# Optimization experiments

Measured on AMD Instinct MI355X. Metric: run time of the kernel, lower is better.

The kernel has to match this reference:

```python
import jax, jax.numpy as jnp
import numpy as np

DIM = 128          # feature dim
HID = 512          # rnn hidden dim
NC = 128           # n_comps (MLP outputs 2*NC)
N = 512            # batch
IN = 2 * DIM + 1   # rnn input size
MLP_H = 4 * HID


def setup_inputs() -> dict:
    key = jax.random.key(0)
    ks = jax.random.split(key, 16)
    s_in = 1.0 / np.sqrt(IN)
    s_h = 1.0 / np.sqrt(HID)
    s_m = 1.0 / np.sqrt(MLP_H)
    f32 = jnp.float32
    return {
        "x": jax.random.normal(ks[0], (N, DIM), f32),
        "mask": jnp.zeros((DIM,), f32),  # all dims unobserved
        # RNN layer 0 (input 2*dim+1 -> hidden)
        "W_ih0": jax.random.uniform(ks[1], (HID, IN), f32, -s_in, s_in),
        "W_hh0": jax.random.uniform(ks[2], (HID, HID), f32, -s_h, s_h),
        "b_ih0": jax.random.uniform(ks[3], (HID,), f32, -s_h, s_h),
        "b_hh0": jax.random.uniform(ks[4], (HID,), f32, -s_h, s_h),
        # RNN layer 1 (hidden -> hidden)
        "W_ih1": jax.random.uniform(ks[5], (HID, HID), f32, -s_h, s_h),
        "W_hh1": jax.random.uniform(ks[6], (HID, HID), f32, -s_h, s_h),
        "b_ih1": jax.random.uniform(ks[7], (HID,), f32, -s_h, s_h),
        "b_hh1": jax.random.uniform(ks[8], (HID,), f32, -s_h, s_h),
        # MLP: hidden -> 4*hidden -> 2*n_comps (ReLU)
        "W1": jax.random.uniform(ks[9], (MLP_H, HID), f32, -s_h, s_h),
        "b1": jax.random.uniform(ks[10], (MLP_H,), f32, -s_h, s_h),
        "W2": jax.random.uniform(ks[11], (2 * NC, MLP_H), f32, -s_m, s_m),
        "b2": jax.random.uniform(ks[12], (2 * NC,), f32, -s_m, s_m),
    }


def _log_prob(xt, means, covs):
    # xt: [N,1], means/covs: [N,NC]
    prec = jax.lax.rsqrt(jax.nn.softplus(covs))
    quad = jnp.sum((xt - means) ** 2 / (prec * prec), axis=1, keepdims=True)
    log_det = jnp.sum(jnp.log(prec), axis=1, keepdims=True)
    return -0.5 * (DIM * np.log(2.0 * np.pi) + quad) + log_det


def reference(x, mask, W_ih0, W_hh0, b_ih0, b_hh0, W_ih1, W_hh1, b_ih1, b_hh1,
              W1, b1, W2, b2):
    n = x.shape[0]
    x_o = x * mask                       # [N, DIM]
    masks = jnp.broadcast_to(mask, (n, DIM))
    # mask is all-zeros by construction -> every dim is unobserved, in order
    x_u = x                              # [N, DIM] unobserved values

    # previous unobserved value fed at each step (zeros at step 0)
    prev_seq = jnp.concatenate([jnp.zeros((n, 1), x.dtype), x_u[:, :-1]], axis=1)
    xs = (prev_seq.T[:, :, None], x_u.T[:, :, None])  # each [DIM, N, 1]

    def step(carry, inp):
        h0, h1, p, _ = carry
        prev_col, targ_col = inp
        cat = jnp.concatenate([prev_col, x_o, masks], axis=1)  # [N, 2*DIM+1]
        h0 = jnp.tanh(cat @ W_ih0.T + b_ih0 + h0 @ W_hh0.T + b_hh0)
        h1 = jnp.tanh(h0 @ W_ih1.T + b_ih1 + h1 @ W_hh1.T + b_hh1)
        o = h1                                               # [N, HID]
        hid = jax.nn.relu(o @ W1.T + b1)
        mc = hid @ W2.T + b2                                 # [N, 2*NC]
        means, covs = mc[:, :NC], mc[:, NC:]
        p = p + _log_prob(targ_col, means, covs)
        return (h0, h1, p, o), None

    init = (jnp.zeros((n, HID), x.dtype), jnp.zeros((n, HID), x.dtype),
            jnp.zeros((n, 1), x.dtype), jnp.zeros((n, HID), x.dtype))
    (h0, h1, p, o_last), _ = jax.lax.scan(step, init, xs)
    return o_last[:, None, :], p  # o: [N,1,HID], p: [N,1]
```

## Files before the change

kernel.cpp:

```cpp
#include <hip/hip_runtime.h>

typedef _Float16 f16;
typedef _Float16 f16x8 __attribute__((ext_vector_type(8)));
typedef float    f32x4 __attribute__((ext_vector_type(4)));
typedef unsigned int u32;
typedef u32 u32x4 __attribute__((ext_vector_type(4)));

#define MFMA16(a, b, c) __builtin_amdgcn_mfma_f32_16x16x32_f16((a), (b), (c), 0, 0, 0)

#define HSZ 262144
#define LOGDET_C 235.2482644923962f

__device__ __forceinline__ void ld16_s(u32x4& d, const f16* p) {
    asm volatile("global_load_dwordx4 %0, %1, off sc0 sc1" : "=v"(d) : "v"(p));
}
__device__ __forceinline__ void ldf_n(float& d, const float* p) {
    asm volatile("global_load_dword %0, %1, off" : "=v"(d) : "v"(p));
}
__device__ __forceinline__ void st2_n(f16* p, f16 v) {
    u32 u = (u32)__builtin_bit_cast(unsigned short, v);
    asm volatile("global_store_short %0, %1, off" :: "v"(p), "v"(u) : "memory");
}
__device__ __forceinline__ void st2_s(f16* p, f16 v) {
    u32 u = (u32)__builtin_bit_cast(unsigned short, v);
    asm volatile("global_store_short %0, %1, off sc0 sc1" :: "v"(p), "v"(u) : "memory");
}
__device__ __forceinline__ void sti_s(int* p, int v) {
    asm volatile("global_store_dword %0, %1, off sc0 sc1" :: "v"(p), "v"(v) : "memory");
}
__device__ __forceinline__ int ldi_s(const int* p) {
    int v;
    asm volatile("global_load_dword %0, %1, off sc0 sc1\ns_waitcnt vmcnt(0)"
                 : "=v"(v) : "v"(p) : "memory");
    return v;
}
__device__ __forceinline__ void gl16(const f16* g, char* l) {
    __builtin_amdgcn_global_load_lds(
        (const __attribute__((address_space(1))) u32*)g,
        (__attribute__((address_space(3))) u32*)l, 16, 0, 0);
}
__device__ __forceinline__ float tanh_fast(float x) {
    float e = __builtin_amdgcn_exp2f(x * 2.8853900817779268f);
    return 1.f - 2.f * __builtin_amdgcn_rcpf(e + 1.f);
}

__global__ void k_conv(const float* __restrict__ x, const float* __restrict__ mask,
                       const float* __restrict__ Wih0,
                       const float* __restrict__ b_ih0, const float* __restrict__ b_hh0,
                       const float* __restrict__ Whh0, const float* __restrict__ Wih1,
                       const float* __restrict__ Whh1, const float* __restrict__ W1,
                       const float* __restrict__ W2,
                       f16* __restrict__ A, f16* __restrict__ B1,
                       float* __restrict__ biasv,
                       f16* __restrict__ Whh0h, f16* __restrict__ Wih1h,
                       f16* __restrict__ Whh1h, f16* __restrict__ W1h,
                       f16* __restrict__ W2h, f16* __restrict__ h1all,
                       int* __restrict__ slots, int* __restrict__ xcdtab)
{
    int gid = blockIdx.x * 256 + threadIdx.x;
    {
        int c = gid >> 7, k = gid & 127;
        A[gid]  = (f16)(x[gid] * mask[k]);
        B1[gid] = (f16)Wih0[c * 257 + 1 + k];
    }
    if (gid < 512) {
        float s = b_ih0[gid] + b_hh0[gid];
        const float* wrow = Wih0 + gid * 257 + 129;
        for (int k = 0; k < 128; k++) s += mask[k] * wrow[k];
        biasv[gid] = s;
    }
    for (int i = gid; i < 262144; i += 65536) {
        Whh0h[i] = (f16)Whh0[i];
        Wih1h[i] = (f16)Wih1[i];
        Whh1h[i] = (f16)Whh1[i];
        h1all[i] = (f16)0.f;
    }
    for (int i = gid; i < 1048576; i += 65536) W1h[i] = (f16)W1[i];
    for (int i = gid; i < 524288;  i += 65536) W2h[i] = (f16)W2[i];
    if (gid < 32768) slots[gid] = 0;
    if (gid < 4096)  xcdtab[gid] = -1;
}

__global__ __launch_bounds__(256) void k_base(const f16* __restrict__ A,
                                              const f16* __restrict__ B1,
                                              const float* __restrict__ biasv,
                                              float* __restrict__ base,
                                              f16* __restrict__ h0s0)
{
    __shared__ float part[4][32][32];
    int tid = threadIdx.x;
    int w = tid >> 6, l = tid & 63;
    int R0 = (blockIdx.x >> 4) * 32, C0 = (blockIdx.x & 15) * 32;
    int lr = l & 15, hi = l >> 4;

    const f16* a0p = A  + (R0 + lr) * 128 + w * 32 + hi * 8;
    const f16* b0p = B1 + (C0 + lr) * 128 + w * 32 + hi * 8;
    f16x8 a0 = *(const f16x8*)(a0p);
    f16x8 a1 = *(const f16x8*)(a0p + 16 * 128);
    f16x8 b0 = *(const f16x8*)(b0p);
    f16x8 b1 = *(const f16x8*)(b0p + 16 * 128);
    f32x4 z = {0.f, 0.f, 0.f, 0.f};
    f32x4 acc00 = MFMA16(a0, b0, z);
    f32x4 acc01 = MFMA16(a0, b1, z);
    f32x4 acc10 = MFMA16(a1, b0, z);
    f32x4 acc11 = MFMA16(a1, b1, z);
#pragma unroll
    for (int r = 0; r < 4; r++) {
        part[w][hi * 4 + r][lr]           = acc00[r];
        part[w][hi * 4 + r][16 + lr]      = acc01[r];
        part[w][16 + hi * 4 + r][lr]      = acc10[r];
        part[w][16 + hi * 4 + r][16 + lr] = acc11[r];
    }
    __syncthreads();
    int rr = tid >> 3, c0 = (tid & 7) * 4;
    int gr = R0 + rr;
#pragma unroll
    for (int cc = 0; cc < 4; cc++) {
        int gc = C0 + c0 + cc;
        float s = part[0][rr][c0 + cc] + part[1][rr][c0 + cc] +
                  part[2][rr][c0 + cc] + part[3][rr][c0 + cc] + biasv[gc];
        base[gr * 512 + gc] = s;
        h0s0[gr * 512 + gc] = (f16)tanh_fast(s);
    }
}

#define LDH(off, f) (*(const f16x8*)((char*)Wl + (off) + lrowB + \
        ((((f) * 64 + hi16)) ^ lswz)))
#define LDB(m, f) (*(const f16x8*)((char*)Wl + \
        (((m) * 32768 + colL * 1024 + (f) * 64 + hi16) ^ cswz)))

#define RNN_STAGED(ST2x)                                                      \
    for (int p = 0; p < 128; p++) {                                           \
        const f16* H0 = h0all + (size_t)(p & PMASK) * HSZ;                    \
        const f16* H1 = h1all + (size_t)p * HSZ;                              \
        f16* H1o = h1all + (size_t)(p + 1) * HSZ;                             \
        f16* H0o = h0all + (size_t)((p + 1) & PMASK) * HSZ;                   \
        float xprev[4];                                                       \
        _Pragma("unroll")                                                     \
        for (int r = 0; r < 4; r++) ldf_n(xprev[r], x + (outrow + r) * 128 + p); \
        if (p) { int v; for (;;) { v = ldi_s(pollB); if (__all(v >= p)) break; \
                                   __builtin_amdgcn_s_sleep(1); } }           \
        _Pragma("unroll")                                                     \
        for (int i = 0; i < 8; i++) {                                         \
            int rr = w * 8 + i;                                               \
            gl16(H0 + (size_t)(R0 + rr) * 512 + ((l ^ (rr & 7)) * 8),         \
                 (char*)Wl + OFF_H0S + rr * 1024);                            \
        }                                                                     \
        asm volatile("s_waitcnt vmcnt(0)" ::: "memory");                      \
        __syncthreads();                                                      \
        f32x4 z4 = {0.f, 0.f, 0.f, 0.f};                                      \
        f32x4 a0a = z4, a0b = z4, a1a = z4, a1b = z4;                         \
        _Pragma("unroll")                                                     \
        for (int f = 0; f < 16; f += 2) {                                     \
            f16x8 A0 = LDH(OFF_H0S, f);                                       \
            f16x8 A1 = LDH(OFF_H0S, f + 1);                                   \
            a0a = MFMA16(A0, bW0[f],     a0a);                                \
            a0b = MFMA16(A1, bW0[f + 1], a0b);                                \
            a1a = MFMA16(A0, LDB(0, f),     a1a);                             \
            a1b = MFMA16(A1, LDB(0, f + 1), a1b);                             \
        }                                                                     \
        f32x4 acc0 = a0a + a0b;                                               \
        _Pragma("unroll")                                                     \
        for (int r = 0; r < 4; r++) {                                         \
            f16 v0 = (f16)tanh_fast(acc0[r] + basef[r] + xprev[r] * w0);      \
            ST2x(H0o + (outrow + r) * 512 + outcolg, v0);                     \
        }                                                                     \
        asm volatile("s_waitcnt vmcnt(0)" ::: "memory");                      \
        if (l == 0) sti_s(myB, p + 1);                                        \
        if (p) { int v; for (;;) { v = ldi_s(pollA); if (__all(v >= p)) break; \
                                   __builtin_amdgcn_s_sleep(1); } }           \
        _Pragma("unroll")                                                     \
        for (int i = 0; i < 8; i++) {                                         \
            int rr = w * 8 + i;                                               \
            gl16(H1 + (size_t)(R0 + rr) * 512 + ((l ^ (rr & 7)) * 8),         \
                 (char*)Wl + OFF_H1S + rr * 1024);                            \
        }                                                                     \
        asm volatile("s_waitcnt vmcnt(0)" ::: "memory");                      \
        __syncthreads();                                                      \
        _Pragma("unroll")                                                     \
        for (int f = 0; f < 16; f += 2) {                                     \
            f16x8 A0 = LDH(OFF_H1S, f);                                       \
            f16x8 A1 = LDH(OFF_H1S, f + 1);                                   \
            a1a = MFMA16(A0, LDB(1, f),     a1a);                             \
            a1b = MFMA16(A1, LDB(1, f + 1), a1b);                             \
        }                                                                     \
        f32x4 acc1 = a1a + a1b;                                               \
        _Pragma("unroll")                                                     \
        for (int r = 0; r < 4; r++) {                                         \
            f16 v1 = (f16)tanh_fast(acc1[r] + bsum);                          \
            ST2x(H1o + (outrow + r) * 512 + outcolg, v1);                     \
        }                                                                     \
        asm volatile("s_waitcnt vmcnt(0)" ::: "memory");                      \
        if (l == 0) sti_s(myA, p + 1);                                        \
    }

#define RNN_DIRECT()                                                          \
    for (int p = 0; p < 128; p++) {                                           \
        const f16* H0 = h0all + (size_t)(p & PMASK) * HSZ;                    \
        const f16* H1 = h1all + (size_t)p * HSZ;                              \
        const f16* ap = H0 + (R0 + r_lo + lr) * 512 + hi * 8;                 \
        const f16* bp = H1 + (R0 + r_lo + lr) * 512 + hi * 8;                 \
        f16* H1o = h1all + (size_t)(p + 1) * HSZ;                             \
        f16* H0o = h0all + (size_t)((p + 1) & PMASK) * HSZ;                   \
        float xprev[4];                                                       \
        _Pragma("unroll")                                                     \
        for (int r = 0; r < 4; r++) ldf_n(xprev[r], x + (outrow + r) * 128 + p); \
        if (p) { int v; for (;;) { v = ldi_s(pollB); if (__all(v >= p)) break; \
                                   __builtin_amdgcn_s_sleep(1); } }           \
        u32x4 ra0[16], ra1[16];                                               \
        __builtin_amdgcn_sched_barrier(0);                                    \
        _Pragma("unroll")                                                     \
        for (int f = 0; f < 16; f++) ld16_s(ra0[f], ap + f * 32);             \
        asm volatile("s_waitcnt vmcnt(0)" ::: "memory");                      \
        __builtin_amdgcn_sched_barrier(0);                                    \
        f32x4 z4 = {0.f, 0.f, 0.f, 0.f};                                      \
        f32x4 a0a = z4, a0b = z4, a1a = z4, a1b = z4;                         \
        _Pragma("unroll")                                                     \
        for (int f = 0; f < 16; f += 2) {                                     \
            f16x8 A0 = __builtin_bit_cast(f16x8, ra0[f]);                     \
            f16x8 A1 = __builtin_bit_cast(f16x8, ra0[f + 1]);                 \
            a0a = MFMA16(A0, bW0[f],     a0a);                                \
            a0b = MFMA16(A1, bW0[f + 1], a0b);                                \
            a1a = MFMA16(A0, LDB(0, f),     a1a);                             \
            a1b = MFMA16(A1, LDB(0, f + 1), a1b);                             \
        }                                                                     \
        f32x4 acc0 = a0a + a0b;                                               \
        _Pragma("unroll")                                                     \
        for (int r = 0; r < 4; r++) {                                         \
            f16 v0 = (f16)tanh_fast(acc0[r] + basef[r] + xprev[r] * w0);      \
            st2_s(H0o + (outrow + r) * 512 + outcolg, v0);                    \
        }                                                                     \
        asm volatile("s_waitcnt vmcnt(0)" ::: "memory");                      \
        if (l == 0) sti_s(myB, p + 1);                                        \
        if (p) { int v; for (;;) { v = ldi_s(pollA); if (__all(v >= p)) break; \
                                   __builtin_amdgcn_s_sleep(1); } }           \
        __builtin_amdgcn_sched_barrier(0);                                    \
        _Pragma("unroll")                                                     \
        for (int f = 0; f < 16; f++) ld16_s(ra1[f], bp + f * 32);             \
        asm volatile("s_waitcnt vmcnt(0)" ::: "memory");                      \
        __builtin_amdgcn_sched_barrier(0);                                    \
        _Pragma("unroll")                                                     \
        for (int f = 0; f < 16; f += 2) {                                     \
            a1a = MFMA16(__builtin_bit_cast(f16x8, ra1[f]),     LDB(1, f),     a1a); \
            a1b = MFMA16(__builtin_bit_cast(f16x8, ra1[f + 1]), LDB(1, f + 1), a1b); \
        }                                                                     \
        f32x4 acc1 = a1a + a1b;                                               \
        _Pragma("unroll")                                                     \
        for (int r = 0; r < 4; r++) {                                         \
            f16 v1 = (f16)tanh_fast(acc1[r] + bsum);                          \
            st2_s(H1o + (outrow + r) * 512 + outcolg, v1);                    \
        }                                                                     \
        asm volatile("s_waitcnt vmcnt(0)" ::: "memory");                      \
        if (l == 0) sti_s(myA, p + 1);                                        \
    }

template<bool H0F>
__global__ __launch_bounds__(256, 1) void k_rnn(
    f16* __restrict__ h0all, f16* __restrict__ h1all,
    const f16* __restrict__ Whh0h, const f16* __restrict__ Wih1h,
    const f16* __restrict__ Whh1h,
    const float* __restrict__ base, const float* __restrict__ x,
    const float* __restrict__ Wih0, const float* __restrict__ b_ih1,
    const float* __restrict__ b_hh1, int* __restrict__ slots,
    int* __restrict__ xcdtab)
{
    constexpr int PMASK = H0F ? 255 : 1;
    const int OFF_H0S = 65536, OFF_H1S = 98304;
    __shared__ __align__(16) char Wl[131072];
    __shared__ int s_fast;
    int tid = threadIdx.x;
    int w = tid >> 6, l = tid & 63;
    int bid = blockIdx.x;
    int sub = (bid >> 3) & 1, cj = bid >> 4;
    int cluster = (bid & 7) * 2 + sub;
    int R0 = cluster * 32, C0 = cj * 32;

    int xcdreg;
    asm("s_getreg_b32 %0, hwreg(20, 0, 4)" : "=s"(xcdreg));
    int my_xcd = xcdreg & 7;
    if (H0F && tid == 0) sti_s(xcdtab + (cluster * 16 + cj) * 16, my_xcd);

    {
        const f16* srcs[2] = { Wih1h, Whh1h };
        for (int m = 0; m < 2; m++) {
            const f16* S = srcs[m] + (size_t)C0 * 512;
            for (int cch = tid; cch < 2048; cch += 256) {
                int col = cch >> 6, kc = cch & 63;
                f16x8 v = *(const f16x8*)(S + col * 512 + kc * 8);
                int byte = m * 32768 + col * 1024 + kc * 16;
                byte ^= (col & 7) << 4;
                *(f16x8*)((char*)Wl + byte) = v;
            }
        }
    }
    __syncthreads();

    int lr = l & 15, hi = l >> 4;
    int r_lo = (w >> 1) * 16, c_lo = (w & 1) * 16;
    int outrow = R0 + r_lo + hi * 4;
    int outcolg = C0 + c_lo + lr;
    int colL = c_lo + lr;
    int lrow = r_lo + lr;
    int lrowB = lrow * 1024;
    int hi16 = hi * 16;
    int lswz = (lrow & 7) << 4;
    int cswz = (colL & 7) << 4;

    f16x8 bW0[16];
    {
        const f16* w0p = Whh0h + (size_t)outcolg * 512 + hi * 8;
#pragma unroll
        for (int f = 0; f < 16; f++) bW0[f] = *(const f16x8*)(w0p + f * 32);
    }

    float basef[4];
#pragma unroll
    for (int r = 0; r < 4; r++) basef[r] = base[(outrow + r) * 512 + outcolg];
    float w0 = Wih0[outcolg * 257];
    float bsum = b_ih1[outcolg] + b_hh1[outcolg];

    int* slotA = slots;
    int* slotB = slots + 16384;
    int wslot = cj * 4 + w;
    int* myA = slotA + (cluster * 64 + wslot) * 16;
    int* myB = slotB + (cluster * 64 + wslot) * 16;
    const int* pollA = slotA + (cluster * 64 + l) * 16;
    const int* pollB = slotB + (cluster * 64 + l) * 16;

    bool fast = false;
    if constexpr (H0F) {
        if (w == 0) {
            int v;
            for (;;) {
                v = (l < 16) ? ldi_s(xcdtab + (cluster * 16 + l) * 16) : 0;
                if (!__any(l < 16 && v == -1)) break;
                __builtin_amdgcn_s_sleep(1);
            }
            int f = __all(l >= 16 || v == my_xcd);
            if (l == 0) s_fast = f;
        }
        __syncthreads();
        fast = (s_fast != 0);
    } else {
        if (tid == 0) s_fast = 0;
        __syncthreads();
    }

    if (H0F && fast) {
        RNN_STAGED(st2_n)
    } else if (H0F) {
        RNN_STAGED(st2_s)
    } else {
        RNN_DIRECT()
    }
}
#undef LDH
#undef LDB

__global__ __launch_bounds__(512, 2) void k_phaseB(const f16* __restrict__ h1all,
                                                   const f16* __restrict__ W1h,
                                                   const f16* __restrict__ W2h,
                                                   const float* __restrict__ b1v,
                                                   const float* __restrict__ b2,
                                                   const float* __restrict__ x,
                                                   float* __restrict__ pcontrib)
{
    __shared__ __align__(16) char Wl[108544];
    const int OFF_W2 = 65536, OFF_HID = 98304;

    int tid = threadIdx.x;
    int wv = tid >> 6, l = tid & 63;
    int lr = l & 15, hi = l >> 4;
    int M0 = blockIdx.x * 128;

    const f16* Hrow = h1all + HSZ + (size_t)(M0 + wv * 16 + lr) * 512;
    f16x8 afrag[16];
#pragma unroll
    for (int ks = 0; ks < 16; ks++)
        afrag[ks] = *(const f16x8*)(Hrow + ks * 32 + hi * 8);

    f32x4 mc[16] = {};

    {
#pragma unroll
        for (int it = 0; it < 4; it++) {
            int idx = it * 512 + tid;
            gl16(W1h + (size_t)(idx & 31) * 512 + (idx >> 5) * 8,
                 Wl + idx * 16);
        }
#pragma unroll
        for (int it = 0; it < 2; it++) {
            int idx = it * 512 + tid;
            gl16(W2h + (size_t)(idx & 255) * 2048 + (idx >> 8) * 8,
                 Wl + OFF_W2 + idx * 16);
        }
    }

    for (int c = 0; c < 64; c++) {
        int p = c & 1;
        __syncthreads();

        if (c + 1 < 64) {
            const int nc = (c + 1) * 32, q = p ^ 1;
#pragma unroll
            for (int it = 0; it < 4; it++) {
                int idx = it * 512 + tid;
                gl16(W1h + (size_t)(nc + (idx & 31)) * 512 + (idx >> 5) * 8,
                     Wl + q * 32768 + idx * 16);
            }
#pragma unroll
            for (int it = 0; it < 2; it++) {
                int idx = it * 512 + tid;
                gl16(W2h + (size_t)(idx & 255) * 2048 + nc + (idx >> 8) * 8,
                     Wl + OFF_W2 + q * 16384 + idx * 16);
            }
        }

        {
            f32x4 s3a = {0.f, 0.f, 0.f, 0.f}, s3b = s3a;
#pragma unroll
            for (int ks = 0; ks < 16; ks++) {
                f16x8 wb0 = *(const f16x8*)(Wl + p * 32768 +
                                            ((ks * 4 + hi) * 32 + lr) * 16);
                f16x8 wb1 = *(const f16x8*)(Wl + p * 32768 +
                                            ((ks * 4 + hi) * 32 + 16 + lr) * 16);
                s3a = MFMA16(afrag[ks], wb0, s3a);
                s3b = MFMA16(afrag[ks], wb1, s3b);
            }
            float bb0 = b1v[c * 32 + lr];
            float bb1 = b1v[c * 32 + 16 + lr];
#pragma unroll
            for (int r = 0; r < 4; r++) {
                int lrow = wv * 16 + hi * 4 + r;
                *(f16*)(Wl + OFF_HID + (lrow * 40 + lr) * 2) =
                    (f16)fmaxf(s3a[r] + bb0, 0.f);
                *(f16*)(Wl + OFF_HID + (lrow * 40 + 16 + lr) * 2) =
                    (f16)fmaxf(s3b[r] + bb1, 0.f);
            }
        }
        __syncthreads();

        {
            f16x8 a = *(const f16x8*)(Wl + OFF_HID +
                                      ((wv * 16 + lr) * 40 + hi * 8) * 2);
#pragma unroll
            for (int cf = 0; cf < 16; cf++) {
                f16x8 b = *(const f16x8*)(Wl + OFF_W2 + p * 16384 +
                                          (hi * 256 + cf * 16 + lr) * 16);
                mc[cf] = MFMA16(a, b, mc[cf]);
            }
        }
    }

    float quad[4] = {}, ls[4] = {}, xt[4];
#pragma unroll
    for (int r = 0; r < 4; r++) {
        int m = M0 + wv * 16 + hi * 4 + r;
        xt[r] = x[(m & 511) * 128 + (m >> 9)];
    }
#pragma unroll
    for (int cf = 0; cf < 8; cf++) {
        int cc = cf * 16 + lr;
        float bm = b2[cc], bc = b2[128 + cc];
#pragma unroll
        for (int r = 0; r < 4; r++) {
            float mean = mc[cf][r] + bm;
            float cov  = mc[cf + 8][r] + bc;
            float sp = log1pf(expf(-fabsf(cov))) + fmaxf(cov, 0.f);
            float d = xt[r] - mean;
            quad[r] += d * d * sp;
            ls[r] += logf(sp);
        }
    }
#pragma unroll
    for (int mm = 1; mm < 16; mm <<= 1)
#pragma unroll
        for (int r = 0; r < 4; r++) {
            quad[r] += __shfl_xor(quad[r], mm, 64);
            ls[r]   += __shfl_xor(ls[r], mm, 64);
        }
    if (lr == 0) {
#pragma unroll
        for (int r = 0; r < 4; r++) {
            int m = M0 + wv * 16 + hi * 4 + r;
            pcontrib[m] = -0.5f * (LOGDET_C + quad[r]) - 0.5f * ls[r];
        }
    }
}

__global__ void k_fin(const f16* __restrict__ h1last,
                      const float* __restrict__ pcontrib, float* __restrict__ out)
{
    int gid = blockIdx.x * 256 + threadIdx.x;
    for (int i = gid; i < HSZ; i += 131072) out[i] = (float)h1last[i];
    if (gid < 512) {
        float s = 0.f;
        for (int tt = 0; tt < 128; tt++) s += pcontrib[tt * 512 + gid];
        out[HSZ + gid] = s;
    }
}

extern "C" void kernel_launch(void* const* d_in, const int* in_sizes, int n_in,
                              void* d_out, int out_size, void* d_ws, size_t ws_size,
                              hipStream_t stream) {
    const float* x     = (const float*)d_in[0];
    const float* mask  = (const float*)d_in[1];
    const float* Wih0  = (const float*)d_in[2];
    const float* Whh0  = (const float*)d_in[3];
    const float* b_ih0 = (const float*)d_in[4];
    const float* b_hh0 = (const float*)d_in[5];
    const float* Wih1  = (const float*)d_in[6];
    const float* Whh1  = (const float*)d_in[7];
    const float* b_ih1 = (const float*)d_in[8];
    const float* b_hh1 = (const float*)d_in[9];
    const float* W1    = (const float*)d_in[10];
    const float* b1    = (const float*)d_in[11];
    const float* W2    = (const float*)d_in[12];
    const float* b2    = (const float*)d_in[13];

    char* ws = (char*)d_ws;
    size_t off = 0;
    auto take = [&](size_t bytes) { char* p = ws + off; off += (bytes + 255) & ~(size_t)255; return p; };
    float* base    = (float*)take(512 * 512 * 4);
    f16* Whh0h     = (f16*)take(HSZ * 2);
    f16* Wih1h     = (f16*)take(HSZ * 2);
    f16* Whh1h     = (f16*)take(HSZ * 2);
    f16* W1h       = (f16*)take(1048576 * 2);
    f16* W2h       = (f16*)take(524288 * 2);
    f16* h0buf     = (f16*)take(2 * HSZ * 2);
    f16* h1all     = (f16*)take((size_t)129 * HSZ * 2);
    float* pcontrib= (float*)take(128 * 512 * 4);
    f16* A         = (f16*)take(65536 * 2);
    f16* B1        = (f16*)take(65536 * 2);
    float* biasv   = (float*)take(512 * 4);
    int* slots     = (int*)take(32768 * 4);
    int* xcdtab    = (int*)take(4096 * 4);
    if (off > ws_size) return;

    const size_t h0all_bytes = (size_t)129 * HSZ * 2;
    bool big = (off + h0all_bytes + 256 <= ws_size);
    f16* h0all = big ? (f16*)take(h0all_bytes) : h0buf;

    k_conv<<<256, 256, 0, stream>>>(x, mask, Wih0, b_ih0, b_hh0, Whh0, Wih1, Whh1,
                                    W1, W2, A, B1, biasv, Whh0h, Wih1h, Whh1h,
                                    W1h, W2h, h1all, slots, xcdtab);
    k_base<<<256, 256, 0, stream>>>(A, B1, biasv, base, h0all);
    if (big)
        k_rnn<true><<<256, 256, 0, stream>>>(h0all, h1all, Whh0h, Wih1h, Whh1h,
                                             base, x, Wih0, b_ih1, b_hh1, slots,
                                             xcdtab);
    else
        k_rnn<false><<<256, 256, 0, stream>>>(h0all, h1all, Whh0h, Wih1h, Whh1h,
                                              base, x, Wih0, b_ih1, b_hh1, slots,
                                              xcdtab);
    k_phaseB<<<512, 512, 0, stream>>>(h1all, W1h, W2h, b1, b2, x, pcontrib);
    k_fin<<<512, 256, 0, stream>>>(h1all + (size_t)128 * HSZ, pcontrib, (float*)d_out);
}
```

Baseline: 747.3 us.

## Merge the per-step h0/h1 staging phases and use a fragment-major LDS layout

Each recurrent step now stages the previous h1 and the h0 tiles into LDS together, behind a single wait and barrier, instead of two separate poll/load/barrier phases. Both layer-1 matmul halves then run back to back after the h0 output is written, which removes one global round-trip and one barrier from the critical path of every step. The LDS layout for weights and hidden states changes from a row-major XOR swizzle to a fragment-major layout, so fragment reads become a plain base plus offset. The risk is that the new layout brings back LDS bank conflicts, and that an extra barrier at the top of each step is now needed to guard buffer reuse.

Result: slower. 830.8 us (+11.2%).

```diff
diff --git a/kernel.cpp b/kernel.cpp
--- a/kernel.cpp
+++ b/kernel.cpp
@@ -124,10 +124,8 @@
     }
 }
 
-#define LDH(off, f) (*(const f16x8*)((char*)Wl + (off) + lrowB + \
-        ((((f) * 64 + hi16)) ^ lswz)))
-#define LDB(m, f) (*(const f16x8*)((char*)Wl + \
-        (((m) * 32768 + colL * 1024 + (f) * 64 + hi16) ^ cswz)))
+#define LDH(off, f) (*(const f16x8*)((char*)Wl + (off) + (f) * 2048 + hbase))
+#define LDB(m, f)   (*(const f16x8*)((char*)Wl + (m) * 32768 + (f) * 2048 + wbase))
 
 #define RNN_STAGED(ST2x)                                                      \
     for (int p = 0; p < 128; p++) {                                           \
@@ -138,26 +136,31 @@
         float xprev[4];                                                       \
         _Pragma("unroll")                                                     \
         for (int r = 0; r < 4; r++) ldf_n(xprev[r], x + (outrow + r) * 128 + p); \
+        if (p) __syncthreads();      \
+        if (p) { int v; for (;;) { v = ldi_s(pollA); if (__all(v >= p)) break; \
+                                   __builtin_amdgcn_s_sleep(1); } }           \
+        _Pragma("unroll")                                                     \
+        for (int i = 0; i < 8; i++) {                                         \
+            int c = w + i * 4, f = c >> 1, rg = c & 1;                        \
+            gl16(H1 + (size_t)(R0 + rg * 16 + (l >> 2)) * 512 + f * 32 + (l & 3) * 8, \
+                 (char*)Wl + OFF_H1S + f * 2048 + rg * 1024);                 \
+        }                                                                     \
         if (p) { int v; for (;;) { v = ldi_s(pollB); if (__all(v >= p)) break; \
                                    __builtin_amdgcn_s_sleep(1); } }           \
         _Pragma("unroll")                                                     \
         for (int i = 0; i < 8; i++) {                                         \
-            int rr = w * 8 + i;                                               \
-            gl16(H0 + (size_t)(R0 + rr) * 512 + ((l ^ (rr & 7)) * 8),         \
-                 (char*)Wl + OFF_H0S + rr * 1024);                            \
+            int c = w + i * 4, f = c >> 1, rg = c & 1;                        \
+            gl16(H0 + (size_t)(R0 + rg * 16 + (l >> 2)) * 512 + f * 32 + (l & 3) * 8, \
+                 (char*)Wl + OFF_H0S + f * 2048 + rg * 1024);                 \
         }                                                                     \
         asm volatile("s_waitcnt vmcnt(0)" ::: "memory");                      \
         __syncthreads();                                                      \
         f32x4 z4 = {0.f, 0.f, 0.f, 0.f};                                      \
-        f32x4 a0a = z4, a0b = z4, a1a = z4, a1b = z4;                         \
+        f32x4 a0a = z4, a0b = z4;                                             \
         _Pragma("unroll")                                                     \
         for (int f = 0; f < 16; f += 2) {                                     \
-            f16x8 A0 = LDH(OFF_H0S, f);                                       \
-            f16x8 A1 = LDH(OFF_H0S, f + 1);                                   \
-            a0a = MFMA16(A0, bW0[f],     a0a);                                \
-            a0b = MFMA16(A1, bW0[f + 1], a0b);                                \
-            a1a = MFMA16(A0, LDB(0, f),     a1a);                             \
-            a1b = MFMA16(A1, LDB(0, f + 1), a1b);                             \
+            a0a = MFMA16(LDH(OFF_H0S, f),     bW0[f],     a0a);               \
+            a0b = MFMA16(LDH(OFF_H0S, f + 1), bW0[f + 1], a0b);               \
         }                                                                     \
         f32x4 acc0 = a0a + a0b;                                               \
         _Pragma("unroll")                                                     \
@@ -165,25 +168,19 @@
             f16 v0 = (f16)tanh_fast(acc0[r] + basef[r] + xprev[r] * w0);      \
             ST2x(H0o + (outrow + r) * 512 + outcolg, v0);                     \
         }                                                                     \
+        f32x4 a1a = z4, a1b = z4;                                             \
+        _Pragma("unroll")                                                     \
+        for (int f = 0; f < 16; f += 2) {                                     \
+            a1a = MFMA16(LDH(OFF_H0S, f),     LDB(0, f),     a1a);            \
+            a1b = MFMA16(LDH(OFF_H0S, f + 1), LDB(0, f + 1), a1b);            \
+        }                                                                     \
+        _Pragma("unroll")                                                     \
+        for (int f = 0; f < 16; f += 2) {                                     \
+            a1a = MFMA16(LDH(OFF_H1S, f),     LDB(1, f),     a1a);            \
+            a1b = MFMA16(LDH(OFF_H1S, f + 1), LDB(1, f + 1), a1b);            \
+        }                                                                     \
         asm volatile("s_waitcnt vmcnt(0)" ::: "memory");                      \
         if (l == 0) sti_s(myB, p + 1);                                        \
-        if (p) { int v; for (;;) { v = ldi_s(pollA); if (__all(v >= p)) break; \
-                                   __builtin_amdgcn_s_sleep(1); } }           \
-        _Pragma("unroll")                                                     \
-        for (int i = 0; i < 8; i++) {                                         \
-            int rr = w * 8 + i;                                               \
-            gl16(H1 + (size_t)(R0 + rr) * 512 + ((l ^ (rr & 7)) * 8),         \
-                 (char*)Wl + OFF_H1S + rr * 1024);                            \
-        }                                                                     \
-        asm volatile("s_waitcnt vmcnt(0)" ::: "memory");                      \
-        __syncthreads();                                                      \
-        _Pragma("unroll")                                                     \
-        for (int f = 0; f < 16; f += 2) {                                     \
-            f16x8 A0 = LDH(OFF_H1S, f);                                       \
-            f16x8 A1 = LDH(OFF_H1S, f + 1);                                   \
-            a1a = MFMA16(A0, LDB(1, f),     a1a);                             \
-            a1b = MFMA16(A1, LDB(1, f + 1), a1b);                             \
-        }                                                                     \
         f32x4 acc1 = a1a + a1b;                                               \
         _Pragma("unroll")                                                     \
         for (int r = 0; r < 4; r++) {                                         \
@@ -282,15 +279,12 @@
 
     {
         const f16* srcs[2] = { Wih1h, Whh1h };
-        for (int m = 0; m < 2; m++) {
-            const f16* S = srcs[m] + (size_t)C0 * 512;
-            for (int cch = tid; cch < 2048; cch += 256) {
-                int col = cch >> 6, kc = cch & 63;
-                f16x8 v = *(const f16x8*)(S + col * 512 + kc * 8);
-                int byte = m * 32768 + col * 1024 + kc * 16;
-                byte ^= (col & 7) << 4;
-                *(f16x8*)((char*)Wl + byte) = v;
-            }
+        for (int ch = tid; ch < 4096; ch += 256) {
+            int m = ch >> 11, c2 = ch & 2047;
+            int col = c2 >> 6, f = (c2 >> 2) & 15, hh = c2 & 3;
+            f16x8 v = *(const f16x8*)(srcs[m] + (size_t)(C0 + col) * 512 +
+                                      f * 32 + hh * 8);
+            *(f16x8*)((char*)Wl + m * 32768 + f * 2048 + col * 64 + hh * 16) = v;
         }
     }
     __syncthreads();
@@ -299,12 +293,8 @@
     int r_lo = (w >> 1) * 16, c_lo = (w & 1) * 16;
     int outrow = R0 + r_lo + hi * 4;
     int outcolg = C0 + c_lo + lr;
-    int colL = c_lo + lr;
-    int lrow = r_lo + lr;
-    int lrowB = lrow * 1024;
-    int hi16 = hi * 16;
-    int lswz = (lrow & 7) << 4;
-    int cswz = (colL & 7) << 4;
+    int hbase = (r_lo + lr) * 64 + hi * 16;
+    int wbase = (c_lo + lr) * 64 + hi * 16;
 
     f16x8 bW0[16];
     {
```

## Assign RNN clusters dynamically by XCD so all blocks of a cluster share one XCD

Applied to the files above, without the earlier changes.

Blocks now publish their XCD id to a table and wait until all 256 entries are filled. If every XCD hosts exactly 32 blocks, each block takes a cluster and column index from its rank among blocks on the same XCD. This keeps all blocks of a cluster on one XCD, so the fast path with non-coherent stores can run instead of depending on the fixed bid mapping happening to line up. The cost is a global all-block handshake at kernel start, and it falls back to the old mapping when the XCD distribution is uneven.

Result: no change. 748.9 us (median of 2 runs) (+0.2%).

```diff
diff --git a/kernel.cpp b/kernel.cpp
--- a/kernel.cpp
+++ b/kernel.cpp
@@ -5,6 +5,7 @@
 typedef float    f32x4 __attribute__((ext_vector_type(4)));
 typedef unsigned int u32;
 typedef u32 u32x4 __attribute__((ext_vector_type(4)));
+typedef unsigned long long u64;
 
 #define MFMA16(a, b, c) __builtin_amdgcn_mfma_f32_16x16x32_f16((a), (b), (c), 0, 0, 0)
 
@@ -127,7 +128,7 @@
 #define LDH(off, f) (*(const f16x8*)((char*)Wl + (off) + lrowB + \
         ((((f) * 64 + hi16)) ^ lswz)))
 #define LDB(m, f) (*(const f16x8*)((char*)Wl + \
-        (((m) * 32768 + colL * 1024 + (f) * 64 + hi16) ^ cswz)))
+        ((((m) * 32768 + colL * 1024 + (f) * 64 + hi16)) ^ cswz)))
 
 #define RNN_STAGED(ST2x)                                                      \
     for (int p = 0; p < 128; p++) {                                           \
@@ -179,10 +180,8 @@
         __syncthreads();                                                      \
         _Pragma("unroll")                                                     \
         for (int f = 0; f < 16; f += 2) {                                     \
-            f16x8 A0 = LDH(OFF_H1S, f);                                       \
-            f16x8 A1 = LDH(OFF_H1S, f + 1);                                   \
-            a1a = MFMA16(A0, LDB(1, f),     a1a);                             \
-            a1b = MFMA16(A1, LDB(1, f + 1), a1b);                             \
+            a1a = MFMA16(LDH(OFF_H1S, f),     LDB(1, f),     a1a);            \
+            a1b = MFMA16(LDH(OFF_H1S, f + 1), LDB(1, f + 1), a1b);            \
         }                                                                     \
         f32x4 acc1 = a1a + a1b;                                               \
         _Pragma("unroll")                                                     \
@@ -267,18 +266,67 @@
     constexpr int PMASK = H0F ? 255 : 1;
     const int OFF_H0S = 65536, OFF_H1S = 98304;
     __shared__ __align__(16) char Wl[131072];
-    __shared__ int s_fast;
+    __shared__ int s_mode, s_cluster, s_cj;
     int tid = threadIdx.x;
     int w = tid >> 6, l = tid & 63;
     int bid = blockIdx.x;
-    int sub = (bid >> 3) & 1, cj = bid >> 4;
-    int cluster = (bid & 7) * 2 + sub;
+
+    int xcdreg;
+    asm("s_getreg_b32 %0, hwreg(20, 0, 32)" : "=s"(xcdreg));
+    int xcc = xcdreg & 7;
+
+    if constexpr (H0F) {
+        if (tid == 0) sti_s(xcdtab + bid * 16, xcc);
+        if (w == 0) {
+            int e[4];
+            for (;;) {
+                bool neg = false;
+#pragma unroll
+                for (int g = 0; g < 4; g++) {
+                    e[g] = ldi_s(xcdtab + (g * 64 + l) * 16);
+                    neg |= (e[g] < 0);
+                }
+                if (!__any(neg)) break;
+                __builtin_amdgcn_s_sleep(1);
+            }
+            int ok = 1;
+#pragma unroll
+            for (int k = 0; k < 8; k++) {
+                int cnt = 0;
+#pragma unroll
+                for (int g = 0; g < 4; g++)
+                    cnt += __popcll(__ballot(e[g] == k));
+                if (cnt != 32) ok = 0;
+            }
+            int rank = 0;
+#pragma unroll
+            for (int g = 0; g < 4; g++) {
+                u64 m = __ballot(e[g] == xcc);
+                int b0 = g * 64;
+                u64 lt = (bid <= b0) ? 0ull
+                       : (bid >= b0 + 64) ? ~0ull
+                       : ((1ull << (bid - b0)) - 1);
+                rank += __popcll(m & lt);
+            }
+            if (l == 0) {
+                s_mode = ok;
+                s_cluster = ok ? (xcc * 2 + (rank >> 4))
+                               : ((bid & 7) * 2 + ((bid >> 3) & 1));
+                s_cj = ok ? (rank & 15) : (bid >> 4);
+            }
+        }
+        __syncthreads();
+    } else {
+        if (tid == 0) {
+            s_mode = 0;
+            s_cluster = (bid & 7) * 2 + ((bid >> 3) & 1);
+            s_cj = bid >> 4;
+        }
+        __syncthreads();
+    }
+    const bool fast = (s_mode != 0);
+    int cluster = s_cluster, cj = s_cj;
     int R0 = cluster * 32, C0 = cj * 32;
-
-    int xcdreg;
-    asm("s_getreg_b32 %0, hwreg(20, 0, 4)" : "=s"(xcdreg));
-    int my_xcd = xcdreg & 7;
-    if (H0F && tid == 0) sti_s(xcdtab + (cluster * 16 + cj) * 16, my_xcd);
 
     {
         const f16* srcs[2] = { Wih1h, Whh1h };
@@ -326,25 +374,6 @@
     int* myB = slotB + (cluster * 64 + wslot) * 16;
     const int* pollA = slotA + (cluster * 64 + l) * 16;
     const int* pollB = slotB + (cluster * 64 + l) * 16;
-
-    bool fast = false;
-    if constexpr (H0F) {
-        if (w == 0) {
-            int v;
-            for (;;) {
-                v = (l < 16) ? ldi_s(xcdtab + (cluster * 16 + l) * 16) : 0;
-                if (!__any(l < 16 && v == -1)) break;
-                __builtin_amdgcn_s_sleep(1);
-            }
-            int f = __all(l >= 16 || v == my_xcd);
-            if (l == 0) s_fast = f;
-        }
-        __syncthreads();
-        fast = (s_fast != 0);
-    } else {
-        if (tid == 0) s_fast = 0;
-        __syncthreads();
-    }
 
     if (H0F && fast) {
         RNN_STAGED(st2_n)
```
